# Kernel optimization log

Hardware: AMD Instinct MI355X
Metric: run time of the kernel (lower is better)

## Reference

```python
import jax, jax.numpy as jnp
import numpy as np

B, D_IN, UNITS, D_OUT = 16384, 1024, 512, 512
T_END = 0.1  # ODE integrated over t in (0, 0.1)


def setup_inputs() -> dict:
    key = jax.random.key(0)
    ks = jax.random.split(key, 8)
    return {
        "x": jax.random.normal(ks[0], (B, D_IN), dtype=jnp.float32),
        "w_in": jax.random.normal(ks[1], (UNITS, D_IN), dtype=jnp.float32) * 0.02,
        "b_in": jax.random.normal(ks[2], (UNITS,), dtype=jnp.float32) * 0.02,
        "sensory_w": jax.random.normal(ks[3], (UNITS, UNITS), dtype=jnp.float32) * 0.1,
        "sensory_sigma": jax.random.normal(ks[4], (UNITS,), dtype=jnp.float32) * 0.1,
        # tau = rand(units)*0.5 + 0.5  (in [0.5, 1.0])
        "tau": jax.random.uniform(ks[5], (UNITS,), dtype=jnp.float32) * 0.5 + 0.5,
        "readout_w": jax.random.normal(ks[6], (D_OUT, UNITS), dtype=jnp.float32) * 0.02,
        "readout_b": jax.random.normal(ks[7], (D_OUT,), dtype=jnp.float32) * 0.02,
        # liquid_state buffer starts at zeros, expanded to batch
        "states": jnp.zeros((B, UNITS), dtype=jnp.float32),
    }


def reference(x, w_in, b_in, sensory_w, sensory_sigma, tau, readout_w, readout_b, states):
    # input projection: tanh(Linear(x))
    projected = jnp.tanh(x @ w_in.T + b_in)                       # [B, U]
    # sensory activation A = sigmoid(projected @ sensory_w + sigma)
    A = jax.nn.sigmoid(projected @ sensory_w + sensory_sigma)     # [B, U]
    # ODE dy/dt = (-y + A)/tau has the closed-form solution
    #   y(t) = A + (y0 - A) * exp(-t / tau)
    # which is exactly what solve_ivp(RK45) approximates at t=0.1.
    decay = jnp.exp(-T_END / tau)                                 # [U]
    new_states = A + (states - A) * decay                         # [B, U]
    # readout
    output = new_states @ readout_w.T + readout_b                 # [B, D_OUT]
    return (output, new_states)
```

## Files before the change

kernel.cpp:

```cpp
#include <hip/hip_runtime.h>
#include <stdint.h>
#include <math.h>

typedef __bf16 bf16;
typedef __bf16 bf16x8 __attribute__((ext_vector_type(8)));
typedef __bf16 bf16x4 __attribute__((ext_vector_type(4)));
typedef float f32x4 __attribute__((ext_vector_type(4)));

static constexpr int BATCH = 16384;
static constexpr int D_IN  = 1024;
static constexpr int UNITS = 512;
static constexpr int D_OUT = 512;

__device__ __forceinline__ void gll16(const void* g, void* l) {
    __builtin_amdgcn_global_load_lds(
        (const __attribute__((address_space(1))) void*)g,
        (__attribute__((address_space(3))) void*)l,
        16, 0, 0);
}

__global__ __launch_bounds__(256)
void k_prep(const float* __restrict__ w_in, const float* __restrict__ sens_w,
            const float* __restrict__ ro_w,
            bf16* __restrict__ w_in_bf, bf16* __restrict__ sensT, bf16* __restrict__ ro_bf)
{
    __shared__ float tile[32][33];
    const int b = blockIdx.x;
    const int t = threadIdx.x;
    if (b < 512) {
        int i = b * 256 + t;
        f32x4 v = ((const f32x4*)w_in)[i];
        bf16x4 o = { (bf16)v.x, (bf16)v.y, (bf16)v.z, (bf16)v.w };
        ((bf16x4*)w_in_bf)[i] = o;
    } else if (b < 768) {
        int bb = b - 512;
        int bx = bb & 15, by = bb >> 4;
        int tx = t & 31, ty = t >> 5;
        #pragma unroll
        for (int j = ty; j < 32; j += 8)
            tile[j][tx] = sens_w[(size_t)(by * 32 + j) * UNITS + bx * 32 + tx];
        __syncthreads();
        #pragma unroll
        for (int j = ty; j < 32; j += 8)
            sensT[(size_t)(bx * 32 + j) * UNITS + by * 32 + tx] = (bf16)tile[tx][j];
    } else {
        int i = (b - 768) * 256 + t;
        f32x4 v = ((const f32x4*)ro_w)[i];
        bf16x4 o = { (bf16)v.x, (bf16)v.y, (bf16)v.z, (bf16)v.w };
        ((bf16x4*)ro_bf)[i] = o;
    }
}

template<int K, int EPI, bool AF32>
__global__ __launch_bounds__(512, 4)
void k_gemm(const float* __restrict__ Af, const bf16* __restrict__ Ab,
            const bf16* __restrict__ Bw,
            const float* __restrict__ bias,
            const float* __restrict__ tau,
            const float* __restrict__ states,
            float* __restrict__ outF, bf16* __restrict__ outB,
            int M, int N)
{
    constexpr int ABPB = AF32 ? (128 * 32 * 4) : (128 * 32 * 2);
    __shared__ __align__(16) char sAraw[2][ABPB];
    __shared__ bf16 sB[2][128 * 32];

    const int t = threadIdx.x;
    const int ntiles = N >> 7;
    const int nwg = gridDim.x;
    const int d = blockIdx.x;
    const int bid = (d & 7) * (nwg >> 3) + (d >> 3);
    const int mtile = bid / ntiles;
    const int ntile = bid % ntiles;
    const int m0 = mtile << 7, n0 = ntile << 7;

    const int lane = t & 63;
    const int wave = t >> 6;
    const int wr = (wave >> 1) * 32;
    const int wc = (wave & 1) * 64;
    const int l15 = lane & 15;
    const int lk  = (lane >> 4) * 8;

    f32x4 acc[2][4];
    #pragma unroll
    for (int m = 0; m < 2; ++m)
        #pragma unroll
        for (int n = 0; n < 4; ++n)
            acc[m][n] = (f32x4){0.f, 0.f, 0.f, 0.f};

    const int brow = t >> 2, bk8 = (t & 3) * 8;
    const bf16* bbp = Bw + (size_t)(n0 + brow) * K + bk8;
    const int ar  = t >> 3;
    const int aqs = (((t & 7) ^ (ar & 7)) << 4);
    const char* ag0 = (const char*)Af + (size_t)(m0 + ar) * K * 4 + aqs;
    const char* ag1 = (const char*)Af + (size_t)(m0 + 64 + ar) * K * 4 + aqs;
    const bf16* abp = Ab + (size_t)(m0 + brow) * K + bk8;

    auto STAGE = [&](int buf, int kt) {
        if constexpr (AF32) {
            gll16(ag0 + (size_t)kt * 4, &sAraw[buf][t * 16]);
            gll16(ag1 + (size_t)kt * 4, &sAraw[buf][8192 + t * 16]);
        } else {
            gll16(abp + kt, &((bf16*)sAraw[buf])[t * 8]);
        }
        gll16(bbp + kt, &sB[buf][t * 8]);
    };

    STAGE(0, 0);
    __syncthreads();

    int cur = 0;
    for (int kt = 0; kt < K; kt += 32) {
        if (kt + 32 < K) STAGE(cur ^ 1, kt + 32);

        bf16x8 afr[2], bfr[4];
        if constexpr (AF32) {
            #pragma unroll
            for (int m = 0; m < 2; ++m) {
                const int r = wr + m * 16 + l15;
                const int s = (r & 7) << 4;
                const char* rb = &sAraw[cur][r * 128];
                f32x4 h0 = *(const f32x4*)(rb + ((lk * 4) ^ s));
                f32x4 h1 = *(const f32x4*)(rb + ((lk * 4 + 16) ^ s));
                afr[m] = (bf16x8){ (bf16)h0.x, (bf16)h0.y, (bf16)h0.z, (bf16)h0.w,
                                   (bf16)h1.x, (bf16)h1.y, (bf16)h1.z, (bf16)h1.w };
            }
        } else {
            #pragma unroll
            for (int m = 0; m < 2; ++m)
                afr[m] = *(const bf16x8*)&((const bf16*)sAraw[cur])[(wr + m * 16 + l15) * 32 + lk];
        }
        #pragma unroll
        for (int n = 0; n < 4; ++n)
            bfr[n] = *(const bf16x8*)&sB[cur][(wc + n * 16 + l15) * 32 + lk];

        #pragma unroll
        for (int m = 0; m < 2; ++m)
            #pragma unroll
            for (int n = 0; n < 4; ++n)
                acc[m][n] = __builtin_amdgcn_mfma_f32_16x16x32_bf16(
                                afr[m], bfr[n], acc[m][n], 0, 0, 0);

        __syncthreads();
        cur ^= 1;
    }

    const int rbase = m0 + wr + ((lane >> 4) << 2);
    const int cbase = n0 + wc + l15;
    #pragma unroll
    for (int n = 0; n < 4; ++n) {
        const int gc = cbase + n * 16;
        const float bv = bias[gc];
        float dec = 0.f;
        if constexpr (EPI == 2) dec = __expf(-0.1f / tau[gc]);
        #pragma unroll
        for (int m = 0; m < 2; ++m) {
            #pragma unroll
            for (int r = 0; r < 4; ++r) {
                const int gr = rbase + m * 16 + r;
                float v = acc[m][n][r] + bv;
                if constexpr (EPI == 1) {
                    float tv = 1.0f - 2.0f / (1.0f + __expf(2.0f * v));
                    outB[(size_t)gr * N + gc] = (bf16)tv;
                } else if constexpr (EPI == 2) {
                    float a = 1.0f / (1.0f + __expf(-v));
                    float s = states[(size_t)gr * N + gc];
                    outF[(size_t)gr * N + gc] = a + (s - a) * dec;
                } else {
                    outF[(size_t)gr * N + gc] = v;
                }
            }
        }
    }
}

extern "C" void kernel_launch(void* const* d_in, const int* in_sizes, int n_in,
                              void* d_out, int out_size, void* d_ws, size_t ws_size,
                              hipStream_t stream) {
    const float* x        = (const float*)d_in[0];
    const float* w_in     = (const float*)d_in[1];
    const float* b_in     = (const float*)d_in[2];
    const float* sens_w   = (const float*)d_in[3];
    const float* sens_sig = (const float*)d_in[4];
    const float* tau      = (const float*)d_in[5];
    const float* ro_w     = (const float*)d_in[6];
    const float* ro_b     = (const float*)d_in[7];
    const float* states   = (const float*)d_in[8];

    float* out    = (float*)d_out;
    float* new_st = out + (size_t)BATCH * D_OUT;
    bf16*  proj   = (bf16*)d_out;

    bf16* w_in_bf = (bf16*)d_ws;
    bf16* sensT   = w_in_bf + (size_t)UNITS * D_IN;
    bf16* ro_bf   = sensT + (size_t)UNITS * UNITS;

    k_prep<<<1024, 256, 0, stream>>>(w_in, sens_w, ro_w, w_in_bf, sensT, ro_bf);

    k_gemm<1024, 1, true><<<(BATCH / 128) * (UNITS / 128), 512, 0, stream>>>(
        x, nullptr, w_in_bf, b_in, nullptr, nullptr, nullptr, proj, BATCH, UNITS);

    k_gemm<512, 2, false><<<(BATCH / 128) * (UNITS / 128), 512, 0, stream>>>(
        nullptr, proj, sensT, sens_sig, tau, states, new_st, nullptr, BATCH, UNITS);

    k_gemm<512, 3, true><<<(BATCH / 128) * (D_OUT / 128), 512, 0, stream>>>(
        new_st, nullptr, ro_bf, ro_b, nullptr, nullptr, out, nullptr, BATCH, D_OUT);
}
```

Baseline: 89.60 us.

## Triple-buffer GEMM K-loop with explicit vmcnt waits and swizzled bf16 LDS tiles

Moves the shared GEMM kernel from double to triple buffering of the A and B LDS tiles. Two stages of global-to-LDS loads stay in flight, and the loop waits with explicit s_waitcnt vmcnt counts and raw barriers instead of __syncthreads. It also XOR-swizzles the bf16 B and A tiles in LDS to cut bank conflicts on fragment reads, and precomputes the LDS read offsets. The goal is to hide global load latency behind MFMA work. In exchange, LDS per block grows to 72KB for the fp32-A path, which may lower occupancy, and each step now has two barriers.

Measured after the change: 79.64 us. 11.1% less time.

```diff
diff --git a/kernel.cpp b/kernel.cpp
--- a/kernel.cpp
+++ b/kernel.cpp
@@ -17,6 +17,18 @@
         (const __attribute__((address_space(1))) void*)g,
         (__attribute__((address_space(3))) void*)l,
         16, 0, 0);
+}
+
+template<int N>
+__device__ __forceinline__ void waitvm() {
+    static_assert(N < 16, "vmcnt imm");
+    __builtin_amdgcn_s_waitcnt(0x0F70 | N);
+    asm volatile("" ::: "memory");
+}
+__device__ __forceinline__ void barrier_raw() {
+    asm volatile("" ::: "memory");
+    __builtin_amdgcn_s_barrier();
+    asm volatile("" ::: "memory");
 }
 
 __global__ __launch_bounds__(256)
@@ -61,9 +73,11 @@
             float* __restrict__ outF, bf16* __restrict__ outB,
             int M, int N)
 {
+    constexpr int NSTEP = K / 32;
+    constexpr int L = AF32 ? 3 : 2;
     constexpr int ABPB = AF32 ? (128 * 32 * 4) : (128 * 32 * 2);
-    __shared__ __align__(16) char sAraw[2][ABPB];
-    __shared__ bf16 sB[2][128 * 32];
+    __shared__ __align__(16) char sAraw[3][ABPB];
+    __shared__ bf16 sB[3][128 * 32];
 
     const int t = threadIdx.x;
     const int ntiles = N >> 7;
@@ -88,62 +102,94 @@
         for (int n = 0; n < 4; ++n)
             acc[m][n] = (f32x4){0.f, 0.f, 0.f, 0.f};
 
-    const int brow = t >> 2, bk8 = (t & 3) * 8;
-    const bf16* bbp = Bw + (size_t)(n0 + brow) * K + bk8;
-    const int ar  = t >> 3;
-    const int aqs = (((t & 7) ^ (ar & 7)) << 4);
-    const char* ag0 = (const char*)Af + (size_t)(m0 + ar) * K * 4 + aqs;
-    const char* ag1 = (const char*)Af + (size_t)(m0 + 64 + ar) * K * 4 + aqs;
-    const bf16* abp = Ab + (size_t)(m0 + brow) * K + bk8;
+    const int brow = t >> 2;
+    const int bslot8 = ((t & 3) ^ ((brow >> 1) & 3)) * 8;
+    const bf16* bbp = Bw + (size_t)(n0 + brow) * K + bslot8;
+    const bf16* abp = AF32 ? nullptr : (Ab + (size_t)(m0 + brow) * K + bslot8);
+    const int ar = t >> 3;
+    const int aslot16 = ((t & 7) ^ (ar & 7)) * 16;
+    const char* ag0 = (const char*)Af + (size_t)(m0 + ar) * K * 4 + aslot16;
+    const char* ag1 = (const char*)Af + (size_t)(m0 + 64 + ar) * K * 4 + aslot16;
 
     auto STAGE = [&](int buf, int kt) {
         if constexpr (AF32) {
             gll16(ag0 + (size_t)kt * 4, &sAraw[buf][t * 16]);
             gll16(ag1 + (size_t)kt * 4, &sAraw[buf][8192 + t * 16]);
         } else {
-            gll16(abp + kt, &((bf16*)sAraw[buf])[t * 8]);
-        }
-        gll16(bbp + kt, &sB[buf][t * 8]);
+            gll16(abp + kt, &sAraw[buf][t * 16]);
+        }
+        gll16(bbp + kt, (char*)&sB[buf][0] + t * 16);
     };
 
-    STAGE(0, 0);
-    __syncthreads();
-
-    int cur = 0;
-    for (int kt = 0; kt < K; kt += 32) {
-        if (kt + 32 < K) STAGE(cur ^ 1, kt + 32);
-
+    int offB[4];
+    #pragma unroll
+    for (int n = 0; n < 4; ++n) {
+        const int R = wc + n * 16 + l15;
+        offB[n] = R * 64 + ((lk * 2) ^ (((R >> 1) & 3) << 4));
+    }
+    int offA0[2], offA1[2];
+    #pragma unroll
+    for (int m = 0; m < 2; ++m) {
+        const int R = wr + m * 16 + l15;
+        if constexpr (AF32) {
+            const int s = (R & 7) << 4;
+            offA0[m] = R * 128 + ((lk * 4) ^ s);
+            offA1[m] = R * 128 + ((lk * 4 + 16) ^ s);
+        } else {
+            offA0[m] = R * 64 + ((lk * 2) ^ (((R >> 1) & 3) << 4));
+        }
+    }
+
+    auto COMPUTE = [&](int buf) {
+        const char* aB = &sAraw[buf][0];
+        const char* bB = (const char*)&sB[buf][0];
         bf16x8 afr[2], bfr[4];
         if constexpr (AF32) {
             #pragma unroll
             for (int m = 0; m < 2; ++m) {
-                const int r = wr + m * 16 + l15;
-                const int s = (r & 7) << 4;
-                const char* rb = &sAraw[cur][r * 128];
-                f32x4 h0 = *(const f32x4*)(rb + ((lk * 4) ^ s));
-                f32x4 h1 = *(const f32x4*)(rb + ((lk * 4 + 16) ^ s));
+                f32x4 h0 = *(const f32x4*)(aB + offA0[m]);
+                f32x4 h1 = *(const f32x4*)(aB + offA1[m]);
                 afr[m] = (bf16x8){ (bf16)h0.x, (bf16)h0.y, (bf16)h0.z, (bf16)h0.w,
                                    (bf16)h1.x, (bf16)h1.y, (bf16)h1.z, (bf16)h1.w };
             }
         } else {
             #pragma unroll
             for (int m = 0; m < 2; ++m)
-                afr[m] = *(const bf16x8*)&((const bf16*)sAraw[cur])[(wr + m * 16 + l15) * 32 + lk];
+                afr[m] = *(const bf16x8*)(aB + offA0[m]);
         }
         #pragma unroll
         for (int n = 0; n < 4; ++n)
-            bfr[n] = *(const bf16x8*)&sB[cur][(wc + n * 16 + l15) * 32 + lk];
-
+            bfr[n] = *(const bf16x8*)(bB + offB[n]);
         #pragma unroll
         for (int m = 0; m < 2; ++m)
             #pragma unroll
             for (int n = 0; n < 4; ++n)
                 acc[m][n] = __builtin_amdgcn_mfma_f32_16x16x32_bf16(
                                 afr[m], bfr[n], acc[m][n], 0, 0, 0);
-
-        __syncthreads();
-        cur ^= 1;
-    }
+    };
+
+    STAGE(0, 0);
+    STAGE(1, 32);
+    STAGE(2, 64);
+
+    int buf = 0;
+    int kt_stage = 96;
+    for (int i = 0; i < NSTEP - 2; ++i) {
+        waitvm<2 * L>();
+        barrier_raw();
+        COMPUTE(buf);
+        barrier_raw();
+        if (kt_stage < K) { STAGE(buf, kt_stage); kt_stage += 32; }
+        buf = (buf == 2) ? 0 : buf + 1;
+    }
+    waitvm<L>();
+    barrier_raw();
+    COMPUTE(buf);
+    buf = (buf == 2) ? 0 : buf + 1;
+    waitvm<0>();
+    barrier_raw();
+    COMPUTE(buf);
+    asm volatile("" ::: "memory");
 
     const int rbase = m0 + wr + ((lane >> 4) << 2);
     const int cbase = n0 + wc + l15;
```
